# Kernel optimization log

Hardware: AMD Instinct MI355X
Metric: run time of the kernel (lower is better)

Reference implementation:

```python
import jax, jax.numpy as jnp
import numpy as np

B, N, F_IN, H, OUT = 64, 1024, 195, 128, 64
K1, K2 = N // 2, N // 4  # ceil(0.5*N), ceil(0.5*K1)
EPS = 1e-5


def setup_inputs() -> dict:
    key = jax.random.key(0)
    ks = jax.random.split(key, 16)
    rn = lambda k, s: jax.random.normal(k, s, dtype=jnp.float32) * 0.1
    inp = {
        "input": jax.random.normal(ks[0], (B, N, F_IN), dtype=jnp.float32),
        # SAGEConv1 (195->128): lin_l (neighbors, w/ bias), lin_r (root, no bias)
        "W1l": rn(ks[1], (H, F_IN)), "b1l": jnp.zeros((H,), jnp.float32),
        "W1r": rn(ks[2], (H, F_IN)),
        # SAGPooling1 GNN = GraphConv(128->1): lin_rel (sum aggr, w/ bias), lin_root (no bias)
        "Wp1_rel": rn(ks[3], (1, H)), "bp1_rel": jnp.zeros((1,), jnp.float32),
        "Wp1_root": rn(ks[4], (1, H)),
        # SAGEConv2 (128->64)
        "W2l": rn(ks[5], (OUT, H)), "b2l": jnp.zeros((OUT,), jnp.float32),
        "W2r": rn(ks[6], (OUT, H)),
        # SAGPooling2 GNN = GraphConv(64->1)
        "Wp2_rel": rn(ks[7], (1, OUT)), "bp2_rel": jnp.zeros((1,), jnp.float32),
        "Wp2_root": rn(ks[8], (1, OUT)),
        # MLP head
        "fc1_w": rn(ks[9], (512, OUT)), "fc1_b": jnp.zeros((512,), jnp.float32),
        "bn1_g": jnp.ones((512,), jnp.float32), "bn1_b": jnp.zeros((512,), jnp.float32),
        "bn1_m": jnp.zeros((512,), jnp.float32), "bn1_v": jnp.ones((512,), jnp.float32),
        "fc2_w": rn(ks[10], (256, 512)), "fc2_b": jnp.zeros((256,), jnp.float32),
        "bn2_g": jnp.ones((256,), jnp.float32), "bn2_b": jnp.zeros((256,), jnp.float32),
        "bn2_m": jnp.zeros((256,), jnp.float32), "bn2_v": jnp.ones((256,), jnp.float32),
        "fc3_w": rn(ks[11], (2, 256)), "fc3_b": jnp.zeros((2,), jnp.float32),
    }
    return inp


def _corr_adj(x):
    # Pearson corrcoef over rows of x [B,N,F] -> boolean adjacency [B,N,N] (corr > 0.5)
    xc = x - x.mean(axis=-1, keepdims=True)
    cov = jnp.einsum("bnf,bmf->bnm", xc, xc)
    d = jnp.sqrt(jnp.clip(jnp.einsum("bnnf->bn", cov[..., None] * 0 + 0) + jnp.diagonal(cov, axis1=1, axis2=2), 1e-12))
    corr = cov / (d[:, :, None] * d[:, None, :])
    return (corr > 0.5).astype(x.dtype)  # symmetric, includes self-loops


def _sage(x, A, Wl, bl, Wr):
    # PyG SAGEConv: lin_l(mean_{j in N(i)} x_j) + lin_r(x_i)
    deg = A.sum(axis=-1, keepdims=True)
    agg = jnp.einsum("bnm,bmf->bnf", A, x) / jnp.maximum(deg, 1.0)
    return jnp.einsum("bnf,hf->bnh", agg, Wl) + bl + jnp.einsum("bnf,hf->bnh", x, Wr)


def _sagpool(x, A, Wrel, brel, Wroot, k):
    # score via GraphConv (sum aggr): lin_rel(sum_j x_j) + lin_root(x_i)
    agg = jnp.einsum("bnm,bmf->bnf", A, x)
    score = (jnp.einsum("bnf,of->bno", agg, Wrel) + brel
             + jnp.einsum("bnf,of->bno", x, Wroot))[..., 0]  # [B,N]
    top_s, idx = jax.lax.top_k(score, k)  # per-graph top-k nodes
    x_new = jnp.take_along_axis(x, idx[:, :, None], axis=1) * jnp.tanh(top_s)[:, :, None]
    A_new = jnp.take_along_axis(A, idx[:, :, None], axis=1)
    A_new = jnp.take_along_axis(A_new, idx[:, None, :], axis=2)
    return x_new, A_new


def _bn_eval(x, g, b, m, v):
    return g * (x - m) * jax.lax.rsqrt(v + EPS) + b


def reference(input, W1l, b1l, W1r, Wp1_rel, bp1_rel, Wp1_root,
              W2l, b2l, W2r, Wp2_rel, bp2_rel, Wp2_root,
              fc1_w, fc1_b, bn1_g, bn1_b, bn1_m, bn1_v,
              fc2_w, fc2_b, bn2_g, bn2_b, bn2_m, bn2_v,
              fc3_w, fc3_b):
    A = _corr_adj(input)                                   # [B,N,N]
    x = jax.nn.relu(_sage(input, A, W1l, b1l, W1r))        # [B,N,128]
    x, A = _sagpool(x, A, Wp1_rel, bp1_rel, Wp1_root, K1)  # [B,K1,128]
    x = jax.nn.relu(_sage(x, A, W2l, b2l, W2r))            # [B,K1,64]
    x, A = _sagpool(x, A, Wp2_rel, bp2_rel, Wp2_root, K2)  # [B,K2,64]
    x = x.mean(axis=1)                                     # global mean pool -> [B,64]
    x = _bn_eval(jax.nn.relu(x @ fc1_w.T + fc1_b), bn1_g, bn1_b, bn1_m, bn1_v)
    x = _bn_eval(jax.nn.relu(x @ fc2_w.T + fc2_b), bn2_g, bn2_b, bn2_m, bn2_v)
    x = x @ fc3_w.T + fc3_b
    return jax.nn.softmax(x, axis=1)
```

## Files before the change

### kernel.cpp

```cpp
#include <hip/hip_runtime.h>
#include <cstdint>


typedef __bf16 bf16x8 __attribute__((ext_vector_type(8)));
typedef float  floatx4 __attribute__((ext_vector_type(4)));

#define MFMA_BF16(a, b, c) __builtin_amdgcn_mfma_f32_16x16x32_bf16((a), (b), (c), 0, 0, 0)

static constexpr int BATCH = 64, NNODE = 1024, FIN = 195, FPAD = 224;
static constexpr int HD = 128, OD = 64, KP1 = 512, KP2 = 256;

static constexpr size_t OFF_GHI   = 0;
static constexpr size_t OFF_GLO   = 8388608;
static constexpr size_t OFF_A1B   = 16777216;
static constexpr size_t OFF_YR2   = 18874368;
static constexpr size_t OFF_X2    = 35651584;
static constexpr size_t OFF_XHI   = 0;
static constexpr size_t OFF_XLO   = 29360128;
static constexpr size_t OFF_ABITS = 58720256;
static constexpr size_t OFF_X1    = 67108864;
static constexpr size_t OFF_P1    = 100663296;
static constexpr size_t OFF_Q1    = OFF_P1 + 262144;
static constexpr size_t OFF_S1    = OFF_Q1 + 262144;
static constexpr size_t OFF_IDX1  = OFF_S1 + 262144;
static constexpr size_t OFF_GATE1 = OFF_IDX1 + 131072;
static constexpr size_t OFF_P2    = OFF_GATE1 + 131072;
static constexpr size_t OFF_Q2    = OFF_P2 + 131072;
static constexpr size_t OFF_S2    = OFF_Q2 + 131072;
static constexpr size_t OFF_IDX2  = OFF_S2 + 131072;
static constexpr size_t OFF_GATE2 = OFF_IDX2 + 65536;
static constexpr size_t OFF_W1HI  = OFF_GATE2 + 65536;
static constexpr size_t OFF_W1LO  = OFF_W1HI + 114688;
static constexpr size_t OFF_W2HI  = OFF_W1LO + 114688;
static constexpr size_t OFF_W2LO  = OFF_W2HI + 32768;
static constexpr size_t OFF_XHAT  = 102760448;
static constexpr size_t OFF_YR1   = 102760448;

__global__ __launch_bounds__(256) void prep_pack_kernel(
    const float* __restrict__ x, __bf16* __restrict__ xhi,
    __bf16* __restrict__ xlo, __bf16* __restrict__ xhat,
    const float* __restrict__ W1l, const float* __restrict__ W1r,
    __bf16* __restrict__ hi1, __bf16* __restrict__ lo1,
    const float* __restrict__ W2l, const float* __restrict__ W2r,
    __bf16* __restrict__ hi2, __bf16* __restrict__ lo2) {
  int bid = blockIdx.x;
  if (bid < 16384) {
    int row  = bid * 4 + (threadIdx.x >> 6);
    int lane = threadIdx.x & 63;
    const float* xr = x + (long)row * FIN;
    float v0 = xr[lane];
    float v1 = xr[lane + 64];
    float v2 = xr[lane + 128];
    float v3 = (lane < FIN - 192) ? xr[lane + 192] : 0.f;
    float s = v0 + v1 + v2 + v3;
#pragma unroll
    for (int o = 32; o; o >>= 1) s += __shfl_xor(s, o);
    float mean = s * (1.f / (float)FIN);
    float c0 = v0 - mean, c1 = v1 - mean, c2 = v2 - mean;
    float c3 = (lane < FIN - 192) ? (v3 - mean) : 0.f;
    float ss = c0 * c0 + c1 * c1 + c2 * c2 + c3 * c3;
#pragma unroll
    for (int o = 32; o; o >>= 1) ss += __shfl_xor(ss, o);
    float inv = rsqrtf(fmaxf(ss, 1e-12f));
    long base = (long)row * FPAD;
    auto st = [&](int slot, float xv, float cv) {
      __bf16 h = (__bf16)xv;
      xhi[base + slot] = h;
      xlo[base + slot] = (__bf16)(xv - (float)h);
      xhat[base + slot] = (__bf16)(cv * inv);
    };
    st(lane, v0, c0);
    st(lane + 64, v1, c1);
    st(lane + 128, v2, c2);
    if (lane + 192 < FPAD) st(lane + 192, (lane < FIN - 192) ? v3 : 0.f, c3);
  } else if (bid < 16384 + 224) {
    int idx = (bid - 16384) * 256 + threadIdx.x;
    int h = idx / FPAD, k = idx % FPAD;
    float v = 0.f;
    if (k < FIN) v = (h < HD) ? W1l[h * FIN + k] : W1r[(h - HD) * FIN + k];
    __bf16 a = (__bf16)v;
    hi1[idx] = a;
    lo1[idx] = (__bf16)(v - (float)a);
  } else {
    int idx = (bid - 16384 - 224) * 256 + threadIdx.x;
    int h = idx / HD, k = idx % HD;
    float v = (h < OD) ? W2l[h * HD + k] : W2r[(h - OD) * HD + k];
    __bf16 a = (__bf16)v;
    hi2[idx] = a;
    lo2[idx] = (__bf16)(v - (float)a);
  }
}

static constexpr int CK = 40;
__global__ __launch_bounds__(256) void corr_kernel(
    const __bf16* __restrict__ xhat, unsigned short* __restrict__ Abits) {
  __shared__ __align__(16) __bf16 sI[128 * CK];
  __shared__ __align__(16) __bf16 sJ[128 * CK];
  int b = blockIdx.y;
  int rem = blockIdx.x, bi = 0;
  while (rem >= 8 - bi) { rem -= 8 - bi; ++bi; }
  int bj = bi + rem;
  int i0 = bi * 128, j0 = bj * 128;
  const __bf16* Xb = xhat + (long)b * NNODE * FPAD;
  int lane = threadIdx.x & 63, wave = threadIdx.x >> 6;
  int wi = (wave >> 1) * 64, wj = (wave & 1) * 64;
  int lr = lane & 15, lk = (lane >> 4) * 8;
  int strow = threadIdx.x & 127;
  int stc = (threadIdx.x >> 7) * 8;
  floatx4 zero = {0.f, 0.f, 0.f, 0.f};
  floatx4 acc[4][4];
#pragma unroll
  for (int i = 0; i < 4; ++i)
#pragma unroll
    for (int j = 0; j < 4; ++j) acc[i][j] = zero;
  for (int kk = 0; kk < 7; ++kk) {
    int k0 = kk * 32;
    __syncthreads();
    {
      const __bf16* gI = Xb + (long)(i0 + strow) * FPAD + k0;
      const __bf16* gJ = Xb + (long)(j0 + strow) * FPAD + k0;
      *(uint4*)&sI[strow * CK + stc]      = *(const uint4*)(gI + stc);
      *(uint4*)&sI[strow * CK + stc + 16] = *(const uint4*)(gI + stc + 16);
      *(uint4*)&sJ[strow * CK + stc]      = *(const uint4*)(gJ + stc);
      *(uint4*)&sJ[strow * CK + stc + 16] = *(const uint4*)(gJ + stc + 16);
    }
    __syncthreads();
    bf16x8 af[4], bf[4];
#pragma unroll
    for (int t = 0; t < 4; ++t) {
      af[t] = *(const bf16x8*)&sI[(wi + t * 16 + lr) * CK + lk];
      bf[t] = *(const bf16x8*)&sJ[(wj + t * 16 + lr) * CK + lk];
    }
#pragma unroll
    for (int ti = 0; ti < 4; ++ti)
#pragma unroll
      for (int tj = 0; tj < 4; ++tj)
        acc[ti][tj] = MFMA_BF16(af[ti], bf[tj], acc[ti][tj]);
  }
#pragma unroll
  for (int ti = 0; ti < 4; ++ti)
#pragma unroll
    for (int tj = 0; tj < 4; ++tj) {
      floatx4 a = acc[ti][tj];
      unsigned long long m0 = __ballot(a[0] > 0.5f);
      unsigned long long m1 = __ballot(a[1] > 0.5f);
      unsigned long long m2 = __ballot(a[2] > 0.5f);
      unsigned long long m3 = __ballot(a[3] > 0.5f);
      if (lane < 16) {
        unsigned long long mm = (lane & 2) ? ((lane & 1) ? m3 : m2)
                                           : ((lane & 1) ? m1 : m0);
        unsigned short piece = (unsigned short)(mm >> ((lane >> 2) * 16));
        int grow = i0 + wi + ti * 16 + lane;
        int gcol = (j0 + wj + tj * 16) >> 4;
        Abits[((long)b * NNODE + grow) * 64 + gcol] = piece;
      }
    }
}

__global__ __launch_bounds__(256) void transpose_bits_kernel(
    unsigned long long* __restrict__ A64) {
  int blk = blockIdx.x;
  int b = blk / 28, pi = blk % 28;
  int rem = pi, rb = 1;
  while (rem >= rb) { rem -= rb; ++rb; }
  int cb = rem;
  int wave = threadIdx.x >> 6, lane = threadIdx.x & 63;
  int dr = rb * 2 + (wave >> 1);
  int dc = cb * 2 + (wave & 1);
  long base = (long)b * NNODE;
  unsigned long long x = A64[(base + dc * 64 + lane) * 16 + dr];
  const unsigned long long M1  = 0x5555555555555555ULL;
  const unsigned long long M2  = 0x3333333333333333ULL;
  const unsigned long long M4  = 0x0F0F0F0F0F0F0F0FULL;
  const unsigned long long M8  = 0x00FF00FF00FF00FFULL;
  const unsigned long long M16 = 0x0000FFFF0000FFFFULL;
  const unsigned long long M32 = 0x00000000FFFFFFFFULL;
#define TSTEP(K, M)                                                       \
  {                                                                       \
    unsigned long long y = __shfl_xor(x, K);                              \
    x = ((lane & K) == 0) ? ((x & (M)) | ((y & (M)) << K))                \
                          : ((x & ~(M)) | ((y & ~(M)) >> K));             \
  }
  TSTEP(1, M1) TSTEP(2, M2) TSTEP(4, M4) TSTEP(8, M8) TSTEP(16, M16) TSTEP(32, M32)
#undef TSTEP
  A64[(base + dr * 64 + lane) * 16 + dc] = x;
}

__global__ __launch_bounds__(256) void gemm_split_kernel(
    const __bf16* __restrict__ Ahi, const __bf16* __restrict__ Alo,
    const __bf16* __restrict__ Bhi, const __bf16* __restrict__ Blo,
    float* __restrict__ C, int K, int ldc) {
  __shared__ __align__(16) __bf16 sAh[128 * CK], sAl[128 * CK];
  __shared__ __align__(16) __bf16 sBh[128 * CK], sBl[128 * CK];
  long row0 = (long)blockIdx.x * 128;
  int col0 = blockIdx.y * 128;
  int lane = threadIdx.x & 63, wave = threadIdx.x >> 6;
  int wi = (wave >> 1) * 64, wj = (wave & 1) * 64;
  int lr = lane & 15, lk = (lane >> 4) * 8;
  int strow = threadIdx.x & 127;
  int stc = (threadIdx.x >> 7) * 8;
  floatx4 zero = {0.f, 0.f, 0.f, 0.f};
  floatx4 acc[4][4];
#pragma unroll
  for (int i = 0; i < 4; ++i)
#pragma unroll
    for (int j = 0; j < 4; ++j) acc[i][j] = zero;
  int nk = K >> 5;
  for (int kk = 0; kk < nk; ++kk) {
    int k0 = kk * 32;
    __syncthreads();
    {
      const __bf16* gAh = Ahi + (row0 + strow) * K + k0;
      const __bf16* gAl = Alo + (row0 + strow) * K + k0;
      const __bf16* gBh = Bhi + (long)(col0 + strow) * K + k0;
      const __bf16* gBl = Blo + (long)(col0 + strow) * K + k0;
      *(uint4*)&sAh[strow * CK + stc]      = *(const uint4*)(gAh + stc);
      *(uint4*)&sAh[strow * CK + stc + 16] = *(const uint4*)(gAh + stc + 16);
      *(uint4*)&sAl[strow * CK + stc]      = *(const uint4*)(gAl + stc);
      *(uint4*)&sAl[strow * CK + stc + 16] = *(const uint4*)(gAl + stc + 16);
      *(uint4*)&sBh[strow * CK + stc]      = *(const uint4*)(gBh + stc);
      *(uint4*)&sBh[strow * CK + stc + 16] = *(const uint4*)(gBh + stc + 16);
      *(uint4*)&sBl[strow * CK + stc]      = *(const uint4*)(gBl + stc);
      *(uint4*)&sBl[strow * CK + stc + 16] = *(const uint4*)(gBl + stc + 16);
    }
    __syncthreads();
    bf16x8 ah[4], al[4];
#pragma unroll
    for (int t = 0; t < 4; ++t) {
      ah[t] = *(const bf16x8*)&sAh[(wi + t * 16 + lr) * CK + lk];
      al[t] = *(const bf16x8*)&sAl[(wi + t * 16 + lr) * CK + lk];
    }
#pragma unroll
    for (int tj = 0; tj < 4; ++tj) {
      bf16x8 bh = *(const bf16x8*)&sBh[(wj + tj * 16 + lr) * CK + lk];
      bf16x8 bl = *(const bf16x8*)&sBl[(wj + tj * 16 + lr) * CK + lk];
#pragma unroll
      for (int ti = 0; ti < 4; ++ti) {
        acc[ti][tj] = MFMA_BF16(ah[ti], bh, acc[ti][tj]);
        acc[ti][tj] = MFMA_BF16(ah[ti], bl, acc[ti][tj]);
        acc[ti][tj] = MFMA_BF16(al[ti], bh, acc[ti][tj]);
      }
    }
  }
#pragma unroll
  for (int ti = 0; ti < 4; ++ti)
#pragma unroll
    for (int tj = 0; tj < 4; ++tj)
#pragma unroll
      for (int rr = 0; rr < 4; ++rr) {
        long grow = row0 + wi + ti * 16 + (lane >> 4) * 4 + rr;
        int gcol = col0 + wj + tj * 16 + (lane & 15);
        C[grow * ldc + gcol] = acc[ti][tj][rr];
      }
}

__global__ __launch_bounds__(256) void sage1_kernel(
    const unsigned int* __restrict__ Abits32, const float* __restrict__ YR1,
    const float* __restrict__ b1l, const float* __restrict__ Wrel,
    const float* __restrict__ Wroot, float* __restrict__ x1,
    float* __restrict__ p1, float* __restrict__ q1) {
  int half = threadIdx.x >> 7;
  int node = blockIdx.x * 2 + half;
  int b = node >> 10;
  int h = threadIdx.x & 127;
  __shared__ int list[2][1024];
  __shared__ int s_deg[2];
  __shared__ float redp[2][2], redq[2][2];
  if (h < 32) {
    unsigned int word = Abits32[(long)node * 32 + h];
    int cnt = __popc(word);
    int off = cnt;
#pragma unroll
    for (int o = 1; o < 32; o <<= 1) {
      int v = __shfl_up(off, o);
      if (h >= o) off += v;
    }
    off -= cnt;
    if (h == 31) s_deg[half] = off + cnt;
    int basei = h * 32;
    while (word) {
      int t = __ffs(word) - 1;
      word &= word - 1;
      list[half][off++] = basei + t;
    }
  }
  __syncthreads();
  int deg = s_deg[half];
  long ybase = (long)(b << 10) * 256;
  float accv = 0.f;
  for (int d = 0; d < deg; ++d)
    accv += YR1[ybase + (long)list[half][d] * 256 + h];
  float R = YR1[(long)node * 256 + 128 + h];
  float v = accv / (float)(deg < 1 ? 1 : deg) + b1l[h] + R;
  v = fmaxf(v, 0.f);
  x1[(long)node * 128 + h] = v;
  float pv = v * Wrel[h], qv = v * Wroot[h];
#pragma unroll
  for (int o = 32; o; o >>= 1) { pv += __shfl_xor(pv, o); qv += __shfl_xor(qv, o); }
  int wv = h >> 6, lane = h & 63;
  if (lane == 0) { redp[half][wv] = pv; redq[half][wv] = qv; }
  __syncthreads();
  if (h == 0) {
    p1[node] = redp[half][0] + redp[half][1];
    q1[node] = redq[half][0] + redq[half][1];
  }
}

__global__ __launch_bounds__(256) void score_kernel(
    const unsigned int* __restrict__ bits32, const float* __restrict__ p,
    const float* __restrict__ q, const float* __restrict__ brel,
    float* __restrict__ score, int nwords, int rpb_shift) {
  int row = blockIdx.x * 4 + (threadIdx.x >> 6);
  int lane = threadIdx.x & 63;
  int b = row >> rpb_shift;
  const unsigned int* wptr = bits32 + (long)row * nwords;
  const float* pb = p + ((long)b << rpb_shift);
  float s = 0.f;
  if (lane < nwords) {
    unsigned int word = wptr[lane];
    while (word) {
      int t = __ffs(word) - 1;
      word &= word - 1;
      s += pb[lane * 32 + t];
    }
  }
#pragma unroll
  for (int o = 32; o; o >>= 1) s += __shfl_xor(s, o);
  if (lane == 0) score[row] = s + q[row] + brel[0];
}

__global__ void topk_kernel(const float* __restrict__ score, int n, int k,
                            int* __restrict__ idx_out, float* __restrict__ gate_out) {
  int b = blockIdx.x, tid = threadIdx.x;
  float s = score[b * n + tid];
  unsigned int fb = __float_as_uint(s);
  unsigned int key = (fb & 0x80000000u) ? ~fb : (fb | 0x80000000u);
  __shared__ int hist[256];
  __shared__ unsigned int sh_prefix;
  __shared__ int sh_target, cnt_gt, cnt_eq, outpos;
  if (tid == 0) { sh_prefix = 0; sh_target = k; cnt_gt = 0; cnt_eq = 0; outpos = 0; }
  for (int shift = 24; shift >= 0; shift -= 8) {
    if (tid < 256) hist[tid] = 0;
    __syncthreads();
    unsigned int prefix = sh_prefix;
    bool inset = (shift == 24) || ((key >> (shift + 8)) == (prefix >> (shift + 8)));
    if (inset) atomicAdd(&hist[(key >> shift) & 255], 1);
    __syncthreads();
    if (tid < 64) {
      int lane = tid;
      int bb0 = hist[255 - 4 * lane];
      int bb1 = hist[254 - 4 * lane];
      int bb2 = hist[253 - 4 * lane];
      int bb3 = hist[252 - 4 * lane];
      int c0 = bb0, c1 = c0 + bb1, c2 = c1 + bb2, c3 = c2 + bb3;
      int incl = c3;
#pragma unroll
      for (int o = 1; o < 64; o <<= 1) {
        int v = __shfl_up(incl, o);
        if (lane >= o) incl += v;
      }
      int excl = incl - c3;
      int target = sh_target;
      int cum[4] = {excl + c0, excl + c1, excl + c2, excl + c3};
      int prev = excl;
#pragma unroll
      for (int i = 0; i < 4; ++i) {
        if (cum[i] >= target && prev < target) {
          int bin = 255 - (4 * lane + i);
          sh_prefix = prefix | ((unsigned int)bin << shift);
          sh_target = target - prev;
        }
        prev = cum[i];
      }
    }
    __syncthreads();
  }
  unsigned int T = sh_prefix;
  if (key > T) atomicAdd(&cnt_gt, 1);
  __syncthreads();
  int E = k - cnt_gt;
  bool sel = (key > T);
  if (!sel && key == T) sel = (atomicAdd(&cnt_eq, 1) < E);
  if (sel) {
    int posn = atomicAdd(&outpos, 1);
    idx_out[b * k + posn] = tid;
    gate_out[b * k + posn] = tanhf(s);
  }
}

__global__ __launch_bounds__(256) void gather_kernel(
    const float* __restrict__ x1, const int* __restrict__ idx,
    const float* __restrict__ gate, __bf16* __restrict__ ghi,
    __bf16* __restrict__ glo, const unsigned int* __restrict__ Abits32,
    unsigned long long* __restrict__ A1bits) {
  int bid = blockIdx.x;
  if (bid < 16384) {
    long e = (long)bid * 256 + threadIdx.x;
    int h = (int)(e & 127);
    int i = (int)((e >> 7) & 511);
    int b = (int)(e >> 16);
    int srow = idx[(b << 9) + i];
    float v = x1[((long)(b << 10) + srow) * 128 + h] * gate[(b << 9) + i];
    __bf16 a = (__bf16)v;
    ghi[e] = a;
    glo[e] = (__bf16)(v - (float)a);
  } else {
    int gi = (bid - 16384) * 4 + (threadIdx.x >> 6);
    int lane = threadIdx.x & 63;
    int b = gi >> 9;
    int srow = idx[gi];
    const unsigned int* src = Abits32 + ((long)(b << 10) + srow) * 32;
    const int* idxb = idx + (b << 9);
#pragma unroll
    for (int t = 0; t < 8; ++t) {
      int cj = idxb[t * 64 + lane];
      int bit = (src[cj >> 5] >> (cj & 31)) & 1;
      unsigned long long m = __ballot(bit);
      if (lane == 0) A1bits[(long)gi * 8 + t] = m;
    }
  }
}

__global__ __launch_bounds__(256) void sage2_kernel(
    const unsigned int* __restrict__ A1b32, const float* __restrict__ YR2,
    const float* __restrict__ b2l, const float* __restrict__ Wrel,
    const float* __restrict__ Wroot, float* __restrict__ x2,
    float* __restrict__ p2, float* __restrict__ q2) {
  int qw = threadIdx.x >> 6;
  int row = blockIdx.x * 4 + qw;
  int b = row >> 9;
  int h = threadIdx.x & 63;
  __shared__ int list[4][512];
  __shared__ int s_deg[4];
  if (h < 16) {
    unsigned int word = A1b32[(long)row * 16 + h];
    int cnt = __popc(word);
    int off = cnt;
#pragma unroll
    for (int o = 1; o < 16; o <<= 1) {
      int v = __shfl_up(off, o);
      if (h >= o) off += v;
    }
    off -= cnt;
    if (h == 15) s_deg[qw] = off + cnt;
    int basei = h * 32;
    while (word) {
      int t = __ffs(word) - 1;
      word &= word - 1;
      list[qw][off++] = basei + t;
    }
  }
  __syncthreads();
  int deg = s_deg[qw];
  long ybase = (long)(b << 9) * 128;
  float accv = 0.f;
  for (int d = 0; d < deg; ++d)
    accv += YR2[ybase + (long)list[qw][d] * 128 + h];
  float R = YR2[(long)row * 128 + 64 + h];
  float v = fmaxf(accv / (float)(deg < 1 ? 1 : deg) + b2l[h] + R, 0.f);
  x2[(long)row * 64 + h] = v;
  float pv = v * Wrel[h], qv = v * Wroot[h];
#pragma unroll
  for (int o = 32; o; o >>= 1) { pv += __shfl_xor(pv, o); qv += __shfl_xor(qv, o); }
  if (h == 0) { p2[row] = pv; q2[row] = qv; }
}

__global__ __launch_bounds__(512) void head_kernel(
    const float* __restrict__ x2, const int* __restrict__ idx2,
    const float* __restrict__ gate2, const float* __restrict__ fc1_w,
    const float* __restrict__ fc1_b, const float* __restrict__ g1,
    const float* __restrict__ bb1, const float* __restrict__ m1,
    const float* __restrict__ v1, const float* __restrict__ fc2_w,
    const float* __restrict__ fc2_b, const float* __restrict__ g2,
    const float* __restrict__ bb2, const float* __restrict__ m2,
    const float* __restrict__ v2, const float* __restrict__ fc3_w,
    const float* __restrict__ fc3_b, float* __restrict__ out) {
  int b = blockIdx.x, tid = threadIdx.x;
  __shared__ float part[8][64];
  __shared__ float pooled[64];
  __shared__ float h1[512];
  __shared__ float h2[256];
  __shared__ float zz[2];
  int h = tid & 63, grp = tid >> 6;
  float s = 0.f;
  for (int i = grp * 32; i < grp * 32 + 32; ++i) {
    int si = idx2[(b << 8) + i];
    s += x2[((long)(b << 9) + si) * 64 + h] * gate2[(b << 8) + i];
  }
  part[grp][h] = s;
  __syncthreads();
  if (tid < 64) {
    float t = 0.f;
#pragma unroll
    for (int g = 0; g < 8; ++g) t += part[g][tid];
    pooled[tid] = t * (1.f / 256.f);
  }
  __syncthreads();
  {
    float z = fc1_b[tid];
    for (int j = 0; j < 64; ++j) z += pooled[j] * fc1_w[tid * 64 + j];
    z = fmaxf(z, 0.f);
    h1[tid] = g1[tid] * (z - m1[tid]) * rsqrtf(v1[tid] + 1e-5f) + bb1[tid];
  }
  __syncthreads();
  if (tid < 256) {
    float z = fc2_b[tid];
    for (int j = 0; j < 512; ++j) z += h1[j] * fc2_w[tid * 512 + j];
    z = fmaxf(z, 0.f);
    h2[tid] = g2[tid] * (z - m2[tid]) * rsqrtf(v2[tid] + 1e-5f) + bb2[tid];
  }
  __syncthreads();
  if (tid < 2) {
    float z = fc3_b[tid];
    for (int j = 0; j < 256; ++j) z += h2[j] * fc3_w[tid * 256 + j];
    zz[tid] = z;
  }
  __syncthreads();
  if (tid == 0) {
    float mx = fmaxf(zz[0], zz[1]);
    float e0 = expf(zz[0] - mx), e1 = expf(zz[1] - mx);
    float inv = 1.f / (e0 + e1);
    out[b * 2 + 0] = e0 * inv;
    out[b * 2 + 1] = e1 * inv;
  }
}

extern "C" void kernel_launch(void* const* d_in, const int* in_sizes, int n_in,
                              void* d_out, int out_size, void* d_ws, size_t ws_size,
                              hipStream_t stream) {
  (void)in_sizes; (void)n_in; (void)out_size; (void)ws_size;
  const float* input   = (const float*)d_in[0];
  const float* W1l     = (const float*)d_in[1];
  const float* b1l     = (const float*)d_in[2];
  const float* W1r     = (const float*)d_in[3];
  const float* Wp1_rel = (const float*)d_in[4];
  const float* bp1_rel = (const float*)d_in[5];
  const float* Wp1_root= (const float*)d_in[6];
  const float* W2l     = (const float*)d_in[7];
  const float* b2l     = (const float*)d_in[8];
  const float* W2r     = (const float*)d_in[9];
  const float* Wp2_rel = (const float*)d_in[10];
  const float* bp2_rel = (const float*)d_in[11];
  const float* Wp2_root= (const float*)d_in[12];
  const float* fc1_w   = (const float*)d_in[13];
  const float* fc1_b   = (const float*)d_in[14];
  const float* bn1_g   = (const float*)d_in[15];
  const float* bn1_b   = (const float*)d_in[16];
  const float* bn1_m   = (const float*)d_in[17];
  const float* bn1_v   = (const float*)d_in[18];
  const float* fc2_w   = (const float*)d_in[19];
  const float* fc2_b   = (const float*)d_in[20];
  const float* bn2_g   = (const float*)d_in[21];
  const float* bn2_b   = (const float*)d_in[22];
  const float* bn2_m   = (const float*)d_in[23];
  const float* bn2_v   = (const float*)d_in[24];
  const float* fc3_w   = (const float*)d_in[25];
  const float* fc3_b   = (const float*)d_in[26];

  char* ws = (char*)d_ws;
  __bf16* xhi   = (__bf16*)(ws + OFF_XHI);
  __bf16* xlo   = (__bf16*)(ws + OFF_XLO);
  __bf16* xhat  = (__bf16*)(ws + OFF_XHAT);
  unsigned short* Abits = (unsigned short*)(ws + OFF_ABITS);
  const unsigned int* Abits32 = (const unsigned int*)(ws + OFF_ABITS);
  unsigned long long* A64 = (unsigned long long*)(ws + OFF_ABITS);
  float* YR1    = (float*)(ws + OFF_YR1);
  float* x1     = (float*)(ws + OFF_X1);
  float* p1     = (float*)(ws + OFF_P1);
  float* q1     = (float*)(ws + OFF_Q1);
  float* s1     = (float*)(ws + OFF_S1);
  int*   idx1   = (int*)(ws + OFF_IDX1);
  float* gate1  = (float*)(ws + OFF_GATE1);
  float* p2     = (float*)(ws + OFF_P2);
  float* q2     = (float*)(ws + OFF_Q2);
  float* s2     = (float*)(ws + OFF_S2);
  int*   idx2   = (int*)(ws + OFF_IDX2);
  float* gate2  = (float*)(ws + OFF_GATE2);
  __bf16* w1hi  = (__bf16*)(ws + OFF_W1HI);
  __bf16* w1lo  = (__bf16*)(ws + OFF_W1LO);
  __bf16* w2hi  = (__bf16*)(ws + OFF_W2HI);
  __bf16* w2lo  = (__bf16*)(ws + OFF_W2LO);
  __bf16* ghi   = (__bf16*)(ws + OFF_GHI);
  __bf16* glo   = (__bf16*)(ws + OFF_GLO);
  unsigned long long* A1bits = (unsigned long long*)(ws + OFF_A1B);
  const unsigned int* A1b32  = (const unsigned int*)(ws + OFF_A1B);
  float* YR2    = (float*)(ws + OFF_YR2);
  float* x2     = (float*)(ws + OFF_X2);
  float* out    = (float*)d_out;

  prep_pack_kernel<<<16672, 256, 0, stream>>>(input, xhi, xlo, xhat,
                                              W1l, W1r, w1hi, w1lo,
                                              W2l, W2r, w2hi, w2lo);
  corr_kernel<<<dim3(36, 64), 256, 0, stream>>>(xhat, Abits);
  transpose_bits_kernel<<<64 * 28, 256, 0, stream>>>(A64);
  gemm_split_kernel<<<dim3(512, 2), 256, 0, stream>>>(xhi, xlo, w1hi, w1lo, YR1, 224, 256);
  sage1_kernel<<<32768, 256, 0, stream>>>(Abits32, YR1, b1l, Wp1_rel, Wp1_root, x1, p1, q1);
  score_kernel<<<16384, 256, 0, stream>>>(Abits32, p1, q1, bp1_rel, s1, 32, 10);
  topk_kernel<<<64, 1024, 0, stream>>>(s1, 1024, KP1, idx1, gate1);
  gather_kernel<<<24576, 256, 0, stream>>>(x1, idx1, gate1, ghi, glo, Abits32, A1bits);
  gemm_split_kernel<<<dim3(256, 1), 256, 0, stream>>>(ghi, glo, w2hi, w2lo, YR2, 128, 128);
  sage2_kernel<<<8192, 256, 0, stream>>>(A1b32, YR2, b2l, Wp2_rel, Wp2_root, x2, p2, q2);
  score_kernel<<<8192, 256, 0, stream>>>(A1b32, p2, q2, bp2_rel, s2, 16, 9);
  topk_kernel<<<64, 512, 0, stream>>>(s2, 512, KP2, idx2, gate2);
  head_kernel<<<64, 512, 0, stream>>>(x2, idx2, gate2, fc1_w, fc1_b, bn1_g, bn1_b,
                                      bn1_m, bn1_v, fc2_w, fc2_b, bn2_g, bn2_b,
                                      bn2_m, bn2_v, fc3_w, fc3_b, out);
}
```

Measured before the change: 397.7 us.

## Fold bit transpose into GEMM launch, vectorize prep stores, remap corr grid

The standalone bit-matrix transpose kernel is removed. Its work now runs as extra blocks appended to the first split-bf16 GEMM grid, which saves a launch and lets the two run concurrently. The prep kernel now has each lane handle four contiguous features and write 8-byte vector stores instead of scalar strided stores. The correlation kernel uses a flattened 1D grid remapped so consecutive blocks spread batches across XCDs. A risk is that the GEMM now carries the transpose branch and its shared-memory footprint for those blocks.

```diff
diff --git a/kernel.cpp b/kernel.cpp
--- a/kernel.cpp
+++ b/kernel.cpp
@@ -48,31 +48,38 @@
     int row  = bid * 4 + (threadIdx.x >> 6);
     int lane = threadIdx.x & 63;
     const float* xr = x + (long)row * FIN;
-    float v0 = xr[lane];
-    float v1 = xr[lane + 64];
-    float v2 = xr[lane + 128];
-    float v3 = (lane < FIN - 192) ? xr[lane + 192] : 0.f;
-    float s = v0 + v1 + v2 + v3;
+    int k0 = lane * 4;
+    float v[4];
+#pragma unroll
+    for (int i = 0; i < 4; ++i) v[i] = (k0 + i < FIN) ? xr[k0 + i] : 0.f;
+    float s = v[0] + v[1] + v[2] + v[3];
 #pragma unroll
     for (int o = 32; o; o >>= 1) s += __shfl_xor(s, o);
     float mean = s * (1.f / (float)FIN);
-    float c0 = v0 - mean, c1 = v1 - mean, c2 = v2 - mean;
-    float c3 = (lane < FIN - 192) ? (v3 - mean) : 0.f;
-    float ss = c0 * c0 + c1 * c1 + c2 * c2 + c3 * c3;
+    float c[4], ss = 0.f;
+#pragma unroll
+    for (int i = 0; i < 4; ++i) {
+      c[i] = (k0 + i < FIN) ? (v[i] - mean) : 0.f;
+      ss += c[i] * c[i];
+    }
 #pragma unroll
     for (int o = 32; o; o >>= 1) ss += __shfl_xor(ss, o);
     float inv = rsqrtf(fmaxf(ss, 1e-12f));
-    long base = (long)row * FPAD;
-    auto st = [&](int slot, float xv, float cv) {
-      __bf16 h = (__bf16)xv;
-      xhi[base + slot] = h;
-      xlo[base + slot] = (__bf16)(xv - (float)h);
-      xhat[base + slot] = (__bf16)(cv * inv);
-    };
-    st(lane, v0, c0);
-    st(lane + 64, v1, c1);
-    st(lane + 128, v2, c2);
-    if (lane + 192 < FPAD) st(lane + 192, (lane < FIN - 192) ? v3 : 0.f, c3);
+    if (k0 < FPAD) {
+      __bf16 hi4[4], lo4[4], hat4[4];
+#pragma unroll
+      for (int i = 0; i < 4; ++i) {
+        float xv = (k0 + i < FIN) ? v[i] : 0.f;
+        __bf16 h = (__bf16)xv;
+        hi4[i] = h;
+        lo4[i] = (__bf16)(xv - (float)h);
+        hat4[i] = (__bf16)(c[i] * inv);
+      }
+      long base = (long)row * FPAD + k0;
+      *(uint2*)&xhi[base]  = *(const uint2*)hi4;
+      *(uint2*)&xlo[base]  = *(const uint2*)lo4;
+      *(uint2*)&xhat[base] = *(const uint2*)hat4;
+    }
   } else if (bid < 16384 + 224) {
     int idx = (bid - 16384) * 256 + threadIdx.x;
     int h = idx / FPAD, k = idx % FPAD;
@@ -96,8 +103,11 @@
     const __bf16* __restrict__ xhat, unsigned short* __restrict__ Abits) {
   __shared__ __align__(16) __bf16 sI[128 * CK];
   __shared__ __align__(16) __bf16 sJ[128 * CK];
-  int b = blockIdx.y;
-  int rem = blockIdx.x, bi = 0;
+  int bid = blockIdx.x;
+  int xcd = bid & 7;
+  int m = bid >> 3;
+  int b = xcd + ((m & 7) << 3);
+  int rem = m >> 3, bi = 0;
   while (rem >= 8 - bi) { rem -= 8 - bi; ++bi; }
   int bj = bi + rem;
   int i0 = bi * 128, j0 = bj * 128;
@@ -157,41 +167,42 @@
     }
 }
 
-__global__ __launch_bounds__(256) void transpose_bits_kernel(
-    unsigned long long* __restrict__ A64) {
-  int blk = blockIdx.x;
-  int b = blk / 28, pi = blk % 28;
-  int rem = pi, rb = 1;
-  while (rem >= rb) { rem -= rb; ++rb; }
-  int cb = rem;
-  int wave = threadIdx.x >> 6, lane = threadIdx.x & 63;
-  int dr = rb * 2 + (wave >> 1);
-  int dc = cb * 2 + (wave & 1);
-  long base = (long)b * NNODE;
-  unsigned long long x = A64[(base + dc * 64 + lane) * 16 + dr];
-  const unsigned long long M1  = 0x5555555555555555ULL;
-  const unsigned long long M2  = 0x3333333333333333ULL;
-  const unsigned long long M4  = 0x0F0F0F0F0F0F0F0FULL;
-  const unsigned long long M8  = 0x00FF00FF00FF00FFULL;
-  const unsigned long long M16 = 0x0000FFFF0000FFFFULL;
-  const unsigned long long M32 = 0x00000000FFFFFFFFULL;
-#define TSTEP(K, M)                                                       \
-  {                                                                       \
-    unsigned long long y = __shfl_xor(x, K);                              \
-    x = ((lane & K) == 0) ? ((x & (M)) | ((y & (M)) << K))                \
-                          : ((x & ~(M)) | ((y & ~(M)) >> K));             \
-  }
-  TSTEP(1, M1) TSTEP(2, M2) TSTEP(4, M4) TSTEP(8, M8) TSTEP(16, M16) TSTEP(32, M32)
-#undef TSTEP
-  A64[(base + dr * 64 + lane) * 16 + dc] = x;
-}
-
 __global__ __launch_bounds__(256) void gemm_split_kernel(
     const __bf16* __restrict__ Ahi, const __bf16* __restrict__ Alo,
     const __bf16* __restrict__ Bhi, const __bf16* __restrict__ Blo,
-    float* __restrict__ C, int K, int ldc) {
+    float* __restrict__ C, int K, int ldc, int mblocks,
+    unsigned long long* __restrict__ A64, int ntrans) {
   __shared__ __align__(16) __bf16 sAh[128 * CK], sAl[128 * CK];
   __shared__ __align__(16) __bf16 sBh[128 * CK], sBl[128 * CK];
+  if ((int)blockIdx.x >= mblocks) {
+    int t = ((int)blockIdx.x - mblocks) * gridDim.y + blockIdx.y;
+    if (t >= ntrans) return;
+    int b = t / 28, pi = t % 28;
+    int rem = pi, rb = 1;
+    while (rem >= rb) { rem -= rb; ++rb; }
+    int cb = rem;
+    int wave = threadIdx.x >> 6, lane = threadIdx.x & 63;
+    int dr = rb * 2 + (wave >> 1);
+    int dc = cb * 2 + (wave & 1);
+    long base = (long)b * NNODE;
+    unsigned long long xv = A64[(base + dc * 64 + lane) * 16 + dr];
+    const unsigned long long M1  = 0x5555555555555555ULL;
+    const unsigned long long M2  = 0x3333333333333333ULL;
+    const unsigned long long M4  = 0x0F0F0F0F0F0F0F0FULL;
+    const unsigned long long M8  = 0x00FF00FF00FF00FFULL;
+    const unsigned long long M16 = 0x0000FFFF0000FFFFULL;
+    const unsigned long long M32 = 0x00000000FFFFFFFFULL;
+#define TSTEP(Kk, M)                                                      \
+    {                                                                     \
+      unsigned long long y = __shfl_xor(xv, Kk);                          \
+      xv = ((lane & Kk) == 0) ? ((xv & (M)) | ((y & (M)) << Kk))          \
+                              : ((xv & ~(M)) | ((y & ~(M)) >> Kk));       \
+    }
+    TSTEP(1, M1) TSTEP(2, M2) TSTEP(4, M4) TSTEP(8, M8) TSTEP(16, M16) TSTEP(32, M32)
+#undef TSTEP
+    A64[(base + dr * 64 + lane) * 16 + dc] = xv;
+    return;
+  }
   long row0 = (long)blockIdx.x * 128;
   int col0 = blockIdx.y * 128;
   int lane = threadIdx.x & 63, wave = threadIdx.x >> 6;
@@ -591,14 +602,15 @@
   prep_pack_kernel<<<16672, 256, 0, stream>>>(input, xhi, xlo, xhat,
                                               W1l, W1r, w1hi, w1lo,
                                               W2l, W2r, w2hi, w2lo);
-  corr_kernel<<<dim3(36, 64), 256, 0, stream>>>(xhat, Abits);
-  transpose_bits_kernel<<<64 * 28, 256, 0, stream>>>(A64);
-  gemm_split_kernel<<<dim3(512, 2), 256, 0, stream>>>(xhi, xlo, w1hi, w1lo, YR1, 224, 256);
+  corr_kernel<<<2304, 256, 0, stream>>>(xhat, Abits);
+  gemm_split_kernel<<<dim3(512 + 896, 2), 256, 0, stream>>>(
+      xhi, xlo, w1hi, w1lo, YR1, 224, 256, 512, A64, 1792);
   sage1_kernel<<<32768, 256, 0, stream>>>(Abits32, YR1, b1l, Wp1_rel, Wp1_root, x1, p1, q1);
   score_kernel<<<16384, 256, 0, stream>>>(Abits32, p1, q1, bp1_rel, s1, 32, 10);
   topk_kernel<<<64, 1024, 0, stream>>>(s1, 1024, KP1, idx1, gate1);
   gather_kernel<<<24576, 256, 0, stream>>>(x1, idx1, gate1, ghi, glo, Abits32, A1bits);
-  gemm_split_kernel<<<dim3(256, 1), 256, 0, stream>>>(ghi, glo, w2hi, w2lo, YR2, 128, 128);
+  gemm_split_kernel<<<dim3(256, 1), 256, 0, stream>>>(
+      ghi, glo, w2hi, w2lo, YR2, 128, 128, 256, nullptr, 0);
   sage2_kernel<<<8192, 256, 0, stream>>>(A1b32, YR2, b2l, Wp2_rel, Wp2_root, x2, p2, q2);
   score_kernel<<<8192, 256, 0, stream>>>(A1b32, p2, q2, bp2_rel, s2, 16, 9);
   topk_kernel<<<64, 512, 0, stream>>>(s2, 512, KP2, idx2, gate2);
```

New measurement: 384.9 us. 3.2% less time.
